# Performance work log

Hardware: AMD Instinct MI355X
Metric: run time of the kernel (lower is better)

## Reference

```python
import jax, jax.numpy as jnp
import numpy as np

# ---- fixed configuration (from init_kwargs / sensor='WV3', ratio=4) ----
B, NBANDS, H, W = 4, 8, 512, 512
RATIO = 4
BETA = 0.25
KSIZE = 41                    # MTF kernel size used by gen_mtf
SCALE = 2                     # ceil(ratio / 2), StructuralLoss half-window
MASK_HW = 8                   # half-window used by local_corr_mask
MTF_R = MTF_C = 2             # strided scatter offsets in SpectralLossNocorr
EPS = 1e-20
# WV3 Nyquist gains (one per MS band)
GNYQ = np.asarray([0.325, 0.355, 0.360, 0.350, 0.365, 0.360, 0.335, 0.315])


def gen_mtf_kernel():
    """Per-band Gaussian MTF filter, shape (NBANDS, 1, K, K), sum-normalized."""
    fcut = 1.0 / RATIO
    ax = np.arange(KSIZE) - (KSIZE - 1) / 2.0
    xx, yy = np.meshgrid(ax, ax)
    kerns = []
    for g in GNYQ:
        alpha = np.sqrt(((KSIZE - 1) * (fcut / 2.0)) ** 2 / (-2.0 * np.log(g)))
        k = np.exp(-(xx ** 2 + yy ** 2) / (2.0 * alpha ** 2))
        kerns.append(k / k.sum())
    return np.stack(kerns, axis=0)[:, None].astype(np.float32)


def _boxsum(x, w):
    """Sum over a 2w x 2w sliding window via double cumsum (matches torch ref)."""
    x = jnp.pad(x, ((0, 0), (0, 0), (w, w), (w, w)))
    c = jnp.cumsum(jnp.cumsum(x, axis=-1), axis=-2)
    return (c[..., 2 * w:, 2 * w:] - c[..., :-2 * w, 2 * w:]
            - c[..., 2 * w:, :-2 * w] + c[..., :-2 * w, :-2 * w])


def _xcorr(a, b, w):
    """Local cross-correlation (xcorr_torch). a:(B,Ca,H,W), b:(B,Cb,H,W) broadcast."""
    n = 4.0 * w * w
    da = a - _boxsum(a, w) / n
    db = b - _boxsum(b, w) / n
    s_ab = _boxsum(da * db, w)
    s_aa = _boxsum(da * da, w)
    s_bb = _boxsum(db * db, w)
    return s_ab / (jnp.sqrt(s_aa * s_bb) + EPS)


def _depthconv(x, kern):
    # torch Conv2d(groups=nbands, padding='same') == grouped cross-correlation
    return jax.lax.conv_general_dilated(
        x, kern, (1, 1), 'SAME', feature_group_count=kern.shape[0],
        dimension_numbers=('NCHW', 'OIHW', 'NCHW'))


def _local_corr_mask(inp, kern):
    pan = inp[:, -1:, :, :]          # (B,1,H,W)
    ms = inp[:, :-1, :, :]           # (B,NB,H,W)
    k0 = kern[0:1]                   # first-band MTF kernel (1,1,K,K)
    pad = (KSIZE - 1) // 2
    pan = jnp.pad(pan, ((0, 0), (0, 0), (pad, pad), (pad, pad)), mode='edge')
    pan = jax.lax.conv_general_dilated(
        pan, k0, (1, 1), 'VALID', dimension_numbers=('NCHW', 'OIHW', 'NCHW'))
    return 1.0 - _xcorr(pan, ms, MASK_HW)  # (B,NB,H,W)


def setup_inputs() -> dict:
    key = jax.random.key(0)
    k1, k2, k3 = jax.random.split(key, 3)
    return {
        'outputs': jax.random.normal(k1, (B, NBANDS, H, W), jnp.float32),
        'labels': jax.random.uniform(k2, (B, NBANDS + 1, H, W), jnp.float32),
        'inp': jax.random.uniform(k3, (B, NBANDS + 1, H, W), jnp.float32),
        'mtf_kernel': jnp.asarray(gen_mtf_kernel()),           # frozen param
        'spec_mask': jnp.ones((1, NBANDS, H, W), jnp.float32),  # buffer
    }


def reference(outputs, labels, inp, mtf_kernel, spec_mask):
    # ---- SpectralLossNocorr ----
    x = _depthconv(outputs, mtf_kernel)                      # (B,NB,H,W)
    labels_spec = labels[:, :-1]
    sub = labels_spec[:, :, 2::RATIO, 2::RATIO]              # (B,NB,H/4,W/4)
    y = jnp.zeros_like(x).at[:, :, MTF_R::RATIO, MTF_C::RATIO].set(sub)
    msub = jnp.broadcast_to(spec_mask[:, :, 2::RATIO, 2::RATIO], sub.shape)
    Wm = jnp.zeros_like(x).at[:, :, MTF_R::RATIO, MTF_C::RATIO].set(msub)
    Wm = Wm / jnp.sum(Wm)
    L_spec = jnp.sum(jnp.abs(x * Wm - y * Wm))
    # ---- StructuralLoss (with local_corr_mask threshold) ----
    pan = labels[:, -1:, :, :]
    thr = _local_corr_mask(inp, mtf_kernel)                  # (B,NB,H,W)
    Xc = jnp.maximum(_xcorr(outputs, pan, SCALE), -1.0)      # clamp(min=-1)
    X = 1.0 - Xc
    Y = X * (X > thr)                                        # keep worst pixels
    L_struct = jnp.mean(Y)
    return L_spec + BETA * L_struct
```

## Files before the change

### kernel.cpp

```cpp
#include <hip/hip_runtime.h>
#include <hip/hip_bf16.h>

#define HWSZ   262144
#define IMG    512
#define NBATCH 4
#define NBANDS 8

typedef _Float16 half_t;
typedef _Float16 half2v __attribute__((ext_vector_type(2)));
typedef _Float16 half4v __attribute__((ext_vector_type(4)));
typedef _Float16 half8v __attribute__((ext_vector_type(8)));

__device__ __forceinline__ void blockReduceAtomicAdd(double v, double* target,
                                                     double* red) {
    for (int off = 32; off > 0; off >>= 1) v += __shfl_down(v, off, 64);
    const int wave = threadIdx.x >> 6, lane = threadIdx.x & 63;
    if (lane == 0) red[wave] = v;
    __syncthreads();
    if (threadIdx.x == 0) atomicAdd(target, red[0] + red[1] + red[2] + red[3]);
}

__global__ __launch_bounds__(256) void k_pan_h(const float* __restrict__ inp,
                                               const float* __restrict__ mtf,
                                               float* __restrict__ tmpH) {
    __shared__ float seg[296];
    __shared__ float vrow[41];
    const int tid = threadIdx.x;
    const int b = blockIdx.z, r = blockIdx.y, c0 = blockIdx.x * 256;
    if (tid < 41) vrow[tid] = mtf[20 * 41 + tid] / sqrtf(mtf[20 * 41 + 20]);
    const float* pan = inp + ((long)b * 9 + 8) * HWSZ + (long)r * IMG;
    for (int e = tid; e < 296; e += 256) {
        int c = c0 - 20 + e;
        c = min(max(c, 0), IMG - 1);
        seg[e] = pan[c];
    }
    __syncthreads();
    float s = 0.f;
#pragma unroll
    for (int j = 0; j < 41; ++j) s += vrow[j] * seg[tid + j];
    tmpH[(long)b * HWSZ + (long)r * IMG + c0 + tid] = s;
}

__global__ __launch_bounds__(256) void k_pan_v(const float* __restrict__ tmpH,
                                               const float* __restrict__ mtf,
                                               float* __restrict__ panf) {
    __shared__ float ucol[41];
    const int tid = threadIdx.x;
    const int b = blockIdx.z, r = blockIdx.y, c = blockIdx.x * 256 + tid;
    if (tid < 41) ucol[tid] = mtf[tid * 41 + 20] / sqrtf(mtf[20 * 41 + 20]);
    __syncthreads();
    const float* base = tmpH + (long)b * HWSZ;
    float s = 0.f;
#pragma unroll
    for (int i = 0; i < 41; ++i) {
        int rr = min(max(r - 20 + i, 0), IMG - 1);
        s += ucol[i] * base[(long)rr * IMG + c];
    }
    panf[(long)b * HWSZ + (long)r * IMG + c] = s;
}

template <int W>
__global__ __launch_bounds__(256) void k_da(const float* __restrict__ in,
                                            long inBatchStride,
                                            float* __restrict__ out) {
    constexpr int TS = 32, WIN = 2 * W, NN = 4 * W * W, RE = TS + WIN - 1;
    constexpr int SR = RE;
    constexpr int ST = 33;
    __shared__ float RAW[RE * SR];
    __shared__ float T[RE * ST];
    const int tid = threadIdx.x;
    const int tr0 = blockIdx.y * TS, tc0 = blockIdx.x * TS;
    const float* src = in + (long)blockIdx.z * inBatchStride;
    for (int e = tid; e < RE * RE; e += 256) {
        int r = e / RE, c = e % RE;
        int gr = tr0 - (W - 1) + r, gc = tc0 - (W - 1) + c;
        float v = 0.f;
        if (gr >= 0 && gr < IMG && gc >= 0 && gc < IMG) v = src[(long)gr * IMG + gc];
        RAW[r * SR + c] = v;
    }
    __syncthreads();
    for (int e = tid; e < RE * TS; e += 256) {
        int r = e >> 5, j = e & 31;
        float s = 0.f;
#pragma unroll
        for (int k = 0; k < WIN; ++k) s += RAW[r * SR + j + k];
        T[r * ST + j] = s;
    }
    __syncthreads();
    float* dst = out + (long)blockIdx.z * HWSZ;
    for (int e = tid; e < TS * TS; e += 256) {
        int pr = e >> 5, pc = e & 31;
        float s = 0.f;
#pragma unroll
        for (int k = 0; k < WIN; ++k) s += T[(pr + k) * ST + pc];
        float da = RAW[(pr + W - 1) * SR + (pc + W - 1)] - s * (1.0f / NN);
        dst[(long)(tr0 + pr) * IMG + tc0 + pc] = da;
    }
}

template <int W>
__global__ __launch_bounds__(256) void k_sq(const float* __restrict__ in,
                                            float* __restrict__ out) {
    constexpr int TS = 32, WIN = 2 * W, RE = TS + WIN - 1;
    constexpr int SR = RE, ST = 33;
    __shared__ float RAW[RE * SR];
    __shared__ float T[RE * ST];
    const int tid = threadIdx.x;
    const int tr0 = blockIdx.y * TS, tc0 = blockIdx.x * TS;
    const float* src = in + (long)blockIdx.z * HWSZ;
    for (int e = tid; e < RE * RE; e += 256) {
        int r = e / RE, c = e % RE;
        int gr = tr0 - (W - 1) + r, gc = tc0 - (W - 1) + c;
        float v = 0.f;
        if (gr >= 0 && gr < IMG && gc >= 0 && gc < IMG) v = src[(long)gr * IMG + gc];
        RAW[r * SR + c] = v;
    }
    __syncthreads();
    for (int e = tid; e < RE * TS; e += 256) {
        int r = e >> 5, j = e & 31;
        float s = 0.f;
#pragma unroll
        for (int k = 0; k < WIN; ++k) {
            float v = RAW[r * SR + j + k];
            s += v * v;
        }
        T[r * ST + j] = s;
    }
    __syncthreads();
    float* dst = out + (long)blockIdx.z * HWSZ;
    for (int e = tid; e < TS * TS; e += 256) {
        int pr = e >> 5, pc = e & 31;
        float s = 0.f;
#pragma unroll
        for (int k = 0; k < WIN; ++k) s += T[(pr + k) * ST + pc];
        dst[(long)(tr0 + pr) * IMG + tc0 + pc] = s;
    }
}


template <int W> struct WinDims {
    static constexpr int A  = (W + 3) & ~3;
    static constexpr int NU = A + W + 8;
    static constexpr int NF = (NU + 3) / 4;
    static constexpr int NV = NF * 4;
};

template <int W>
__device__ __forceinline__ void loadRowWin(const float* __restrict__ row, int c0,
                                           float* v) {
    constexpr int A = WinDims<W>::A;
    constexpr int NF = WinDims<W>::NF;
#pragma unroll
    for (int f = 0; f < NF; ++f) {
        const int cb = c0 - A + 4 * f;
        if (cb >= 0 && cb + 3 < IMG) {
            const float4 t = *(const float4*)(row + cb);
            v[4 * f + 0] = t.x; v[4 * f + 1] = t.y;
            v[4 * f + 2] = t.z; v[4 * f + 3] = t.w;
        } else {
#pragma unroll
            for (int u = 0; u < 4; ++u) {
                const int c = cb + u;
                v[4 * f + u] = (c >= 0 && c < IMG) ? row[c] : 0.f;
            }
        }
    }
}

template <int W>
__device__ __forceinline__ void loadRowWinH(const half_t* __restrict__ row, int c0,
                                            float* v) {
    constexpr int A = WinDims<W>::A;
    constexpr int NF = WinDims<W>::NF;
#pragma unroll
    for (int f = 0; f < NF; ++f) {
        const int cb = c0 - A + 4 * f;
        if (cb >= 0 && cb + 3 < IMG) {
            const half4v t = *(const half4v*)(row + cb);
            v[4 * f + 0] = (float)t[0]; v[4 * f + 1] = (float)t[1];
            v[4 * f + 2] = (float)t[2]; v[4 * f + 3] = (float)t[3];
        } else {
#pragma unroll
            for (int u = 0; u < 4; ++u) {
                const int c = cb + u;
                v[4 * f + u] = (c >= 0 && c < IMG) ? (float)row[c] : 0.f;
            }
        }
    }
}

template <int W>
__global__ __launch_bounds__(256) void kDAtile(const float* __restrict__ in,
                                               long sB, long sC,
                                               half_t* __restrict__ out) {
    constexpr int A = WinDims<W>::A;
    constexpr int NV = WinDims<W>::NV;
    constexpr int NRS = 63 + 2 * W;
    constexpr int LP = 65;
    constexpr int NN = 4 * W * W;
    __shared__ float T[NRS * LP];
    const int z = blockIdx.z;
    const int tr0 = blockIdx.y * 64, tc0 = blockIdx.x * 64;
    const float* img = in + (long)(z >> 3) * sB + (long)(z & 7) * sC;

    for (int e = threadIdx.x; e < NRS * 8; e += 256) {
        const int i = e >> 3, cg = e & 7;
        const int gr = tr0 - W + 1 + i;
        float* dst = &T[i * LP + cg * 8];
        if (gr < 0 || gr >= IMG) {
#pragma unroll
            for (int j = 0; j < 8; ++j) dst[j] = 0.f;
            continue;
        }
        float v[NV];
        loadRowWin<W>(img + (long)gr * IMG, tc0 + cg * 8, v);
        float s = 0.f;
#pragma unroll
        for (int k = A - W + 1; k <= A + W; ++k) s += v[k];
        dst[0] = s;
#pragma unroll
        for (int j = 1; j < 8; ++j) {
            s += v[A + W + j] - v[A - W + j];
            dst[j] = s;
        }
    }
    __syncthreads();

    const int c = threadIdx.x & 63, q = threadIdx.x >> 6;
    const int ro0 = q * 16;
    float s = 0.f;
#pragma unroll
    for (int k = 0; k < 2 * W; ++k) s += T[(ro0 + k) * LP + c];
    const float* oz = img + tc0 + c;
    half_t* dz = out + (long)z * HWSZ + tc0 + c;
#pragma unroll
    for (int j = 0; j < 16; ++j) {
        const int r = tr0 + ro0 + j;
        const float o = oz[(long)r * IMG];
        dz[(long)r * IMG] = (half_t)(o - s * (1.0f / NN));
        if (j < 15) s += T[(ro0 + j + 2 * W) * LP + c] - T[(ro0 + j) * LP + c];
    }
}

template <int W>
__device__ __forceinline__ void stageProducts(const half_t* __restrict__ daz,
                                              const float* __restrict__ dsz,
                                              int tr0, int tc0,
                                              unsigned int* L) {
    constexpr int A = WinDims<W>::A;
    constexpr int NU = WinDims<W>::NU;
    constexpr int NV = WinDims<W>::NV;
    constexpr int NRS = 63 + 2 * W;
    constexpr int LP = 65;
    for (int e = threadIdx.x; e < NRS * 8; e += 256) {
        const int i = e >> 3, cg = e & 7;
        const int gr = tr0 - W + 1 + i;
        const int c0 = tc0 + cg * 8;
        unsigned int* dst = L + i * LP + cg * 8;
        if (gr < 0 || gr >= IMG) {
#pragma unroll
            for (int j = 0; j < 8; ++j) dst[j] = 0u;
            continue;
        }
        float va[NV], vs[NV];
        loadRowWinH<W>(daz + (long)gr * IMG, c0, va);
        loadRowWin<W>(dsz + (long)gr * IMG, c0, vs);
        float p1[NV], p2[NV];
#pragma unroll
        for (int k = 0; k < NU; ++k) { p1[k] = va[k] * vs[k]; p2[k] = va[k] * va[k]; }
        float s1 = 0.f, s2 = 0.f;
#pragma unroll
        for (int k = A - W + 1; k <= A + W; ++k) { s1 += p1[k]; s2 += p2[k]; }
#pragma unroll
        for (int j = 0; j < 8; ++j) {
            half2v h;
            h[0] = (half_t)s1; h[1] = (half_t)s2;
            dst[j] = __builtin_bit_cast(unsigned int, h);
            if (j < 7) {
                s1 += p1[A + W + 1 + j] - p1[A - W + 1 + j];
                s2 += p2[A + W + 1 + j] - p2[A - W + 1 + j];
            }
        }
    }
}

__global__ __launch_bounds__(256) void kFusedXY(const half_t* __restrict__ daMS,
                                                const float* __restrict__ daPAN,
                                                const float* __restrict__ saa,
                                                const half_t* __restrict__ daOUT,
                                                const float* __restrict__ dbPAN,
                                                const float* __restrict__ sbb,
                                                double* __restrict__ acc) {
    constexpr int LP = 65;
    constexpr int NRS8 = 63 + 16;
    __shared__ unsigned int L[NRS8 * LP];
    __shared__ double red[4];
    const int z = blockIdx.z, b = z >> 3;
    const int tr0 = blockIdx.y * 64, tc0 = blockIdx.x * 64;
    const int c = threadIdx.x & 63, q = threadIdx.x >> 6;
    const int ro0 = q * 16;

    float thrv[16];
    {
        constexpr int W = 8;
        stageProducts<W>(daMS + (long)z * HWSZ, daPAN + (long)b * HWSZ,
                         tr0, tc0, L);
        __syncthreads();
        float s1 = 0.f, s2 = 0.f;
#pragma unroll
        for (int k = 0; k < 2 * W; ++k) {
            const half2v h = __builtin_bit_cast(half2v, L[(ro0 + k) * LP + c]);
            s1 += (float)h[0]; s2 += (float)h[1];
        }
        const float* sz = saa + (long)b * HWSZ + tc0 + c;
#pragma unroll
        for (int j = 0; j < 16; ++j) {
            const int r = tr0 + ro0 + j;
            const float sa = sz[(long)r * IMG];
            const float den = sqrtf(fmaxf(sa * s2, 0.f)) + 1e-20f;
            thrv[j] = 1.0f - s1 / den;
            if (j < 15) {
                const half2v ha = __builtin_bit_cast(half2v, L[(ro0 + j + 2 * W) * LP + c]);
                const half2v hs = __builtin_bit_cast(half2v, L[(ro0 + j) * LP + c]);
                s1 += (float)ha[0] - (float)hs[0];
                s2 += (float)ha[1] - (float)hs[1];
            }
        }
        __syncthreads();
    }
    double ysum = 0.0;
    {
        constexpr int W = 2;
        stageProducts<W>(daOUT + (long)z * HWSZ, dbPAN + (long)b * HWSZ,
                         tr0, tc0, L);
        __syncthreads();
        float s1 = 0.f, s2 = 0.f;
#pragma unroll
        for (int k = 0; k < 2 * W; ++k) {
            const half2v h = __builtin_bit_cast(half2v, L[(ro0 + k) * LP + c]);
            s1 += (float)h[0]; s2 += (float)h[1];
        }
        const float* sz = sbb + (long)b * HWSZ + tc0 + c;
#pragma unroll
        for (int j = 0; j < 16; ++j) {
            const float sb = sz[(long)(tr0 + ro0 + j) * IMG];
            const float den = sqrtf(fmaxf(s2 * sb, 0.f)) + 1e-20f;
            const float Xc = s1 / den;
            const float X = 1.0f - fmaxf(Xc, -1.0f);
            if (X > thrv[j]) ysum += (double)X;
            if (j < 15) {
                const half2v ha = __builtin_bit_cast(half2v, L[(ro0 + j + 2 * W) * LP + c]);
                const half2v hs = __builtin_bit_cast(half2v, L[(ro0 + j) * LP + c]);
                s1 += (float)ha[0] - (float)hs[0];
                s2 += (float)ha[1] - (float)hs[1];
            }
        }
    }
    blockReduceAtomicAdd(ysum, acc + 2, red);
}

__global__ __launch_bounds__(256) void k_spec_h(const float* __restrict__ outputs,
                                                const float* __restrict__ mtf,
                                                float* __restrict__ tmpS) {
    __shared__ float vrow[41];
    const int g = blockIdx.x * 256 + threadIdx.x;
    const int q = g & 31, r = (g >> 5) & 511, z = g >> 14;
    const int band = z & 7;
    if (threadIdx.x < 41)
        vrow[threadIdx.x] = mtf[band * 1681 + 20 * 41 + threadIdx.x] /
                            sqrtf(mtf[band * 1681 + 20 * 41 + 20]);
    __syncthreads();
    const float* row = outputs + (long)z * HWSZ + (long)r * IMG;
    float v[56];
#pragma unroll
    for (int f = 0; f < 14; ++f) {
        const int cb = 16 * q - 20 + 4 * f;
        if (cb >= 0 && cb + 3 < IMG) {
            const float4 t = *(const float4*)(row + cb);
            v[4 * f + 0] = t.x; v[4 * f + 1] = t.y;
            v[4 * f + 2] = t.z; v[4 * f + 3] = t.w;
        } else {
#pragma unroll
            for (int u = 0; u < 4; ++u) {
                const int cc = cb + u;
                v[4 * f + u] = (cc >= 0 && cc < IMG) ? row[cc] : 0.f;
            }
        }
    }
    float o[4] = {0.f, 0.f, 0.f, 0.f};
#pragma unroll
    for (int j = 0; j < 41; ++j) {
        const float w = vrow[j];
#pragma unroll
        for (int u = 0; u < 4; ++u) o[u] += w * v[2 + 4 * u + j];
    }
    float* dst = tmpS + ((long)z * IMG + r) * 128 + 4 * q;
    *(float4*)dst = make_float4(o[0], o[1], o[2], o[3]);
}

__global__ __launch_bounds__(256) void k_spec_v(const float* __restrict__ tmpS,
                                                const float* __restrict__ labels,
                                                const float* __restrict__ spec,
                                                const float* __restrict__ mtf,
                                                double* __restrict__ acc) {
    __shared__ double redT[4];
    __shared__ double redM[4];
    __shared__ float ucol[41];
    const int g = blockIdx.x * 256 + threadIdx.x;
    const int q = g & 31, rs = (g >> 5) & 127, z = g >> 12;
    const int b = z >> 3, band = z & 7;
    if (threadIdx.x < 41)
        ucol[threadIdx.x] = mtf[band * 1681 + threadIdx.x * 41 + 20] /
                            sqrtf(mtf[band * 1681 + 20 * 41 + 20]);
    __syncthreads();
    const float* base = tmpS + (long)z * IMG * 128 + 4 * q;
    const int rbase = 4 * rs - 18;
    float o[4] = {0.f, 0.f, 0.f, 0.f};
    if (rbase >= 0 && rbase + 40 < IMG) {
#pragma unroll
        for (int i = 0; i < 41; ++i) {
            const float4 v = *(const float4*)(base + (long)(rbase + i) * 128);
            const float w = ucol[i];
            o[0] += w * v.x; o[1] += w * v.y; o[2] += w * v.z; o[3] += w * v.w;
        }
    } else {
        for (int i = 0; i < 41; ++i) {
            const int r = rbase + i;
            if (r >= 0 && r < IMG) {
                const float4 v = *(const float4*)(base + (long)r * 128);
                const float w = ucol[i];
                o[0] += w * v.x; o[1] += w * v.y; o[2] += w * v.z; o[3] += w * v.w;
            }
        }
    }
    const int gr = 2 + 4 * rs;
    float tsum = 0.f, msum = 0.f;
#pragma unroll
    for (int u = 0; u < 4; ++u) {
        const int gc = 2 + 4 * (4 * q + u);
        const float m = spec[(long)band * HWSZ + (long)gr * IMG + gc];
        const float y = labels[((long)b * 9 + band) * HWSZ + (long)gr * IMG + gc];
        tsum += fabsf(o[u] * m - y * m);
        msum += m;
    }
    blockReduceAtomicAdd((double)tsum, acc + 0, redT);
    blockReduceAtomicAdd((double)msum, acc + 1, redM);
}

__global__ void k_final(const double* __restrict__ acc, float* __restrict__ out) {
    double lspec = acc[0] / acc[1];
    double lstruct = acc[2] / (double)(NBATCH * NBANDS * HWSZ);
    out[0] = (float)(lspec + 0.25 * lstruct);
}

extern "C" void kernel_launch(void* const* d_in, const int* in_sizes, int n_in,
                              void* d_out, int out_size, void* d_ws, size_t ws_size,
                              hipStream_t stream) {
    const float* outputs = (const float*)d_in[0];
    const float* labels  = (const float*)d_in[1];
    const float* inp     = (const float*)d_in[2];
    const float* mtf     = (const float*)d_in[3];
    const float* spec    = (const float*)d_in[4];
    float* out = (float*)d_out;

    const long IMGB = (long)HWSZ;
    char* ws = (char*)d_ws;
    double* acc    = (double*)ws;
    float* panf    = (float*)(ws + 1024);
    float* tmpH    = panf   + NBATCH * IMGB;
    float* da_pan8 = tmpH   + NBATCH * IMGB;
    float* saa8    = da_pan8 + NBATCH * IMGB;
    float* db_pan2 = saa8   + NBATCH * IMGB;
    float* sbb2    = db_pan2 + NBATCH * IMGB;
    float* tmpS    = sbb2   + NBATCH * IMGB;
    half_t* hDA8   = (half_t*)(tmpS + 8 * IMGB);
    half_t* hDA2   = hDA8 + 32 * IMGB;

    hipMemsetAsync(acc, 0, 4 * sizeof(double), stream);

    k_pan_h<<<dim3(2, 512, NBATCH), 256, 0, stream>>>(inp, mtf, tmpH);
    k_pan_v<<<dim3(2, 512, NBATCH), 256, 0, stream>>>(tmpH, mtf, panf);
    k_da<8><<<dim3(16, 16, NBATCH), 256, 0, stream>>>(panf, (long)HWSZ, da_pan8);
    k_sq<8><<<dim3(16, 16, NBATCH), 256, 0, stream>>>(da_pan8, saa8);
    k_da<2><<<dim3(16, 16, NBATCH), 256, 0, stream>>>(labels + 8 * IMGB,
                                                      (long)9 * HWSZ, db_pan2);
    k_sq<2><<<dim3(16, 16, NBATCH), 256, 0, stream>>>(db_pan2, sbb2);

    k_spec_h<<<2048, 256, 0, stream>>>(outputs, mtf, tmpS);
    k_spec_v<<<512, 256, 0, stream>>>(tmpS, labels, spec, mtf, acc);

    kDAtile<8><<<dim3(8, 8, 32), 256, 0, stream>>>(inp, 9 * IMGB, IMGB, hDA8);
    kDAtile<2><<<dim3(8, 8, 32), 256, 0, stream>>>(outputs, 8 * IMGB, IMGB, hDA2);

    kFusedXY<<<dim3(8, 8, 32), 256, 0, stream>>>(hDA8, da_pan8, saa8,
                                                 hDA2, db_pan2, sbb2, acc);

    k_final<<<1, 1, 0, stream>>>(acc, out);
}
```

Measured before the change: 304.1 us.

## Remap tile blocks per XCD and stage both product windows before one barrier

The 3D grids of the tile kernels become a flat 2048-block grid, decoded so that each XCD (block id mod 8) handles four whole images. This is meant to keep halo reuse inside one XCD's L2. kFusedXY now uses two separate LDS buffers, stages both the W=8 and W=2 product windows up front behind a single barrier, and sets a launch-bounds occupancy hint of 4. This removes two barriers and lets the global loads overlap, at the cost of more LDS per block, which may limit occupancy.

```diff
diff --git a/kernel.cpp b/kernel.cpp
--- a/kernel.cpp
+++ b/kernel.cpp
@@ -189,6 +189,14 @@
     }
 }
 
+__device__ __forceinline__ void xcdDecode(int id, int& z, int& tr0, int& tc0) {
+    const int xcd = id & 7, inner = id >> 3;
+    z = (xcd << 2) | (inner >> 6);
+    const int t = inner & 63;
+    tr0 = (t >> 3) * 64;
+    tc0 = (t & 7) * 64;
+}
+
 template <int W>
 __global__ __launch_bounds__(256) void kDAtile(const float* __restrict__ in,
                                                long sB, long sC,
@@ -199,8 +207,8 @@
     constexpr int LP = 65;
     constexpr int NN = 4 * W * W;
     __shared__ float T[NRS * LP];
-    const int z = blockIdx.z;
-    const int tr0 = blockIdx.y * 64, tc0 = blockIdx.x * 64;
+    int z, tr0, tc0;
+    xcdDecode(blockIdx.x, z, tr0, tc0);
     const float* img = in + (long)(z >> 3) * sB + (long)(z & 7) * sC;
 
     for (int e = threadIdx.x; e < NRS * 8; e += 256) {
@@ -284,32 +292,37 @@
     }
 }
 
-__global__ __launch_bounds__(256) void kFusedXY(const half_t* __restrict__ daMS,
-                                                const float* __restrict__ daPAN,
-                                                const float* __restrict__ saa,
-                                                const half_t* __restrict__ daOUT,
-                                                const float* __restrict__ dbPAN,
-                                                const float* __restrict__ sbb,
-                                                double* __restrict__ acc) {
+__global__ __launch_bounds__(256, 4) void kFusedXY(
+    const half_t* __restrict__ daMS,
+    const float* __restrict__ daPAN,
+    const float* __restrict__ saa,
+    const half_t* __restrict__ daOUT,
+    const float* __restrict__ dbPAN,
+    const float* __restrict__ sbb,
+    double* __restrict__ acc) {
     constexpr int LP = 65;
     constexpr int NRS8 = 63 + 16;
-    __shared__ unsigned int L[NRS8 * LP];
+    constexpr int NRS2 = 63 + 4;
+    __shared__ unsigned int L8[NRS8 * LP];
+    __shared__ unsigned int L2b[NRS2 * LP];
     __shared__ double red[4];
-    const int z = blockIdx.z, b = z >> 3;
-    const int tr0 = blockIdx.y * 64, tc0 = blockIdx.x * 64;
+    int z, tr0, tc0;
+    xcdDecode(blockIdx.x, z, tr0, tc0);
+    const int b = z >> 3;
     const int c = threadIdx.x & 63, q = threadIdx.x >> 6;
     const int ro0 = q * 16;
+
+    stageProducts<8>(daMS + (long)z * HWSZ, daPAN + (long)b * HWSZ, tr0, tc0, L8);
+    stageProducts<2>(daOUT + (long)z * HWSZ, dbPAN + (long)b * HWSZ, tr0, tc0, L2b);
+    __syncthreads();
 
     float thrv[16];
     {
         constexpr int W = 8;
-        stageProducts<W>(daMS + (long)z * HWSZ, daPAN + (long)b * HWSZ,
-                         tr0, tc0, L);
-        __syncthreads();
         float s1 = 0.f, s2 = 0.f;
 #pragma unroll
         for (int k = 0; k < 2 * W; ++k) {
-            const half2v h = __builtin_bit_cast(half2v, L[(ro0 + k) * LP + c]);
+            const half2v h = __builtin_bit_cast(half2v, L8[(ro0 + k) * LP + c]);
             s1 += (float)h[0]; s2 += (float)h[1];
         }
         const float* sz = saa + (long)b * HWSZ + tc0 + c;
@@ -320,24 +333,20 @@
             const float den = sqrtf(fmaxf(sa * s2, 0.f)) + 1e-20f;
             thrv[j] = 1.0f - s1 / den;
             if (j < 15) {
-                const half2v ha = __builtin_bit_cast(half2v, L[(ro0 + j + 2 * W) * LP + c]);
-                const half2v hs = __builtin_bit_cast(half2v, L[(ro0 + j) * LP + c]);
+                const half2v ha = __builtin_bit_cast(half2v, L8[(ro0 + j + 2 * W) * LP + c]);
+                const half2v hs = __builtin_bit_cast(half2v, L8[(ro0 + j) * LP + c]);
                 s1 += (float)ha[0] - (float)hs[0];
                 s2 += (float)ha[1] - (float)hs[1];
             }
         }
-        __syncthreads();
     }
     double ysum = 0.0;
     {
         constexpr int W = 2;
-        stageProducts<W>(daOUT + (long)z * HWSZ, dbPAN + (long)b * HWSZ,
-                         tr0, tc0, L);
-        __syncthreads();
         float s1 = 0.f, s2 = 0.f;
 #pragma unroll
         for (int k = 0; k < 2 * W; ++k) {
-            const half2v h = __builtin_bit_cast(half2v, L[(ro0 + k) * LP + c]);
+            const half2v h = __builtin_bit_cast(half2v, L2b[(ro0 + k) * LP + c]);
             s1 += (float)h[0]; s2 += (float)h[1];
         }
         const float* sz = sbb + (long)b * HWSZ + tc0 + c;
@@ -349,8 +358,8 @@
             const float X = 1.0f - fmaxf(Xc, -1.0f);
             if (X > thrv[j]) ysum += (double)X;
             if (j < 15) {
-                const half2v ha = __builtin_bit_cast(half2v, L[(ro0 + j + 2 * W) * LP + c]);
-                const half2v hs = __builtin_bit_cast(half2v, L[(ro0 + j) * LP + c]);
+                const half2v ha = __builtin_bit_cast(half2v, L2b[(ro0 + j + 2 * W) * LP + c]);
+                const half2v hs = __builtin_bit_cast(half2v, L2b[(ro0 + j) * LP + c]);
                 s1 += (float)ha[0] - (float)hs[0];
                 s2 += (float)ha[1] - (float)hs[1];
             }
@@ -489,11 +498,11 @@
     k_spec_h<<<2048, 256, 0, stream>>>(outputs, mtf, tmpS);
     k_spec_v<<<512, 256, 0, stream>>>(tmpS, labels, spec, mtf, acc);
 
-    kDAtile<8><<<dim3(8, 8, 32), 256, 0, stream>>>(inp, 9 * IMGB, IMGB, hDA8);
-    kDAtile<2><<<dim3(8, 8, 32), 256, 0, stream>>>(outputs, 8 * IMGB, IMGB, hDA2);
-
-    kFusedXY<<<dim3(8, 8, 32), 256, 0, stream>>>(hDA8, da_pan8, saa8,
-                                                 hDA2, db_pan2, sbb2, acc);
+    kDAtile<8><<<2048, 256, 0, stream>>>(inp, 9 * IMGB, IMGB, hDA8);
+    kDAtile<2><<<2048, 256, 0, stream>>>(outputs, 8 * IMGB, IMGB, hDA2);
+
+    kFusedXY<<<2048, 256, 0, stream>>>(hDA8, da_pan8, saa8,
+                                       hDA2, db_pan2, sbb2, acc);
 
     k_final<<<1, 1, 0, stream>>>(acc, out);
 }
```

Result: faster. 281.3 us (-7.5%).
